# Optimization experiments

Hardware: AMD Instinct MI355X
Metric: run time of the kernel (lower is better)

## Reference

```python
import jax, jax.numpy as jnp
import numpy as np

Q, M, KLEN, B = 512, 512, 1024, 4
D, H, DH, G = 1024, 16, 64, 4
DG = D // G          # 256
EPS = 1e-6
SCALE = 1.0 / DH ** 0.5


def _group_ln(x, gamma, beta, n_group):
    # x: [L, B, D]; torch std is unbiased (ddof=1); note (x-mean)/(std+eps)
    L, b, d = x.shape
    xg = x.reshape(L, b, n_group, d // n_group)
    mean = xg.mean(-1, keepdims=True)
    std = jnp.std(xg, axis=-1, ddof=1, keepdims=True)
    out = ((xg - mean) / (std + EPS)).reshape(L, b, d)
    return gamma * out + beta


def _rel_shift(x):
    # x: [q, r, b, n]
    q, r = x.shape[0], x.shape[1]
    zero_pad = jnp.zeros((q, 1) + x.shape[2:], x.dtype)
    x_padded = jnp.concatenate([zero_pad, x], axis=1).reshape((r + 1, q) + x.shape[2:])
    return x_padded[1:].reshape(x.shape)


def setup_inputs() -> dict:
    key = jax.random.key(0)
    ks = jax.random.split(key, 14)
    p = lambda k, s: jax.random.normal(k, s, jnp.float32) * 0.02
    w = jax.random.normal(ks[0], (Q, B, D), jnp.float32)
    r = jax.random.normal(ks[1], (KLEN, 1, D), jnp.float32)
    mems = jax.random.normal(ks[2], (M, B, D), jnp.float32)
    r_w_bias = p(ks[3], (H, DH))
    r_r_bias = p(ks[4], (H, DH))
    gamma_q = jnp.ones((D,), jnp.float32); beta_q = jnp.zeros((D,), jnp.float32)
    gamma_kv = jnp.ones((D,), jnp.float32); beta_kv = jnp.zeros((D,), jnp.float32)
    Wq = p(ks[5], (G, DG, DG))       # grouped conv1d k=1: per-group [out,in]
    Wiq = p(ks[6], (DG, D))          # inter_q_net: conv1d groups=1 [out,in]
    Wk = p(ks[7], (D, D))
    Wv = p(ks[8], (D, D))
    Wr = p(ks[9], (G, DG, DG))       # r_net grouped (n_head*d_head == d_model)
    Wintra = p(ks[10], (G, DG, DG))  # intra_linear grouped conv
    Winter = p(ks[11], (DG, D))      # inter_linear nn.Linear weight
    i = jnp.arange(Q)[:, None]
    j = jnp.arange(KLEN)[None, :]
    attn_mask = (j > i + M)[:, :, None]  # [Q, KLEN, 1] bool, True = masked
    return dict(w=w, r=r, r_w_bias=r_w_bias, r_r_bias=r_r_bias, mems=mems,
                gamma_q=gamma_q, beta_q=beta_q, gamma_kv=gamma_kv, beta_kv=beta_kv,
                Wq=Wq, Wiq=Wiq, Wk=Wk, Wv=Wv, Wr=Wr, Wintra=Wintra, Winter=Winter,
                attn_mask=attn_mask)


def reference(w, r, r_w_bias, r_r_bias, mems, gamma_q, beta_q, gamma_kv, beta_kv,
              Wq, Wiq, Wk, Wv, Wr, Wintra, Winter, attn_mask):
    qlen, bsz, _ = w.shape
    rlen = r.shape[0]
    w_norm = _group_ln(w, gamma_q, beta_q, G)                       # [Q,B,D]
    kv = jnp.concatenate([mems, w], axis=0)
    kv_norm = gamma_kv * (kv - kv.mean(-1, keepdims=True)) / (
        jnp.std(kv, axis=-1, ddof=1, keepdims=True) + EPS) + beta_kv  # [K,B,D]

    # grouped 1x1 conv projections == per-group matmuls
    q_intra = jnp.einsum('qbgd,god->qbgo', w_norm.reshape(qlen, bsz, G, DG), Wq)
    q_global = jnp.einsum('qbd,od->qbo', w_norm, Wiq)               # [Q,B,DG]
    head_q = (q_intra + q_global[:, :, None, :]).reshape(qlen, bsz, H, DH)
    klen = kv_norm.shape[0]
    head_k = jnp.einsum('kbd,od->kbo', kv_norm, Wk).reshape(klen, bsz, H, DH)
    head_v = jnp.einsum('kbd,od->kbo', kv_norm, Wv).reshape(klen, bsz, H, DH)
    r_head_k = jnp.einsum('rgd,god->rgo', r[:, 0].reshape(rlen, G, DG), Wr)
    r_head_k = r_head_k.reshape(rlen, H, DH)                        # [R,H,DH]

    AC = jnp.einsum('ibnd,jbnd->ijbn', head_q + r_w_bias, head_k)
    BD = _rel_shift(jnp.einsum('ibnd,jnd->ijbn', head_q + r_r_bias, r_head_k))
    attn_score = (AC + BD) * SCALE                                  # [Q,K,B,H]
    attn_score = jnp.where(attn_mask[:, :, :, None], -jnp.inf, attn_score)
    attn_prob = jax.nn.softmax(attn_score, axis=1)
    attn_vec = jnp.einsum('ijbn,jbnd->ibnd', attn_prob, head_v)
    attn_out = attn_vec.reshape(qlen, bsz, D)

    inter = jnp.einsum('qbd,od->qbo', attn_out, Winter)             # [Q,B,DG]
    intra = jnp.einsum('qbgd,god->qbgo', attn_out.reshape(qlen, bsz, G, DG), Wintra)
    out = (intra + inter[:, :, None, :]).reshape(qlen, bsz, D)
    return w + out
```

## Files before the change

kernel.cpp:

```cpp
#include <hip/hip_runtime.h>
#include <math.h>

#define Q_LEN 512
#define M_LEN 512
#define KL    1024
#define BSZ   4
#define DM    1024
#define NH    16
#define DHD   64
#define NG    4
#define DGRP  256
#define RL    1024
#define LN_EPS 1e-6f
#define ATT_SCALE 0.125f

typedef short s16x8 __attribute__((ext_vector_type(8)));
typedef float f32x4 __attribute__((ext_vector_type(4)));

__device__ __forceinline__ float wave_sum64(float v) {
#pragma unroll
    for (int off = 32; off > 0; off >>= 1) v += __shfl_xor(v, off);
    return v;
}

__device__ __forceinline__ ushort f2bf(float f) {
    unsigned u = __float_as_uint(f);
    unsigned r = (u + 0x7fffu + ((u >> 16) & 1u)) >> 16;
    return (ushort)r;
}
__device__ __forceinline__ float bf2f(ushort u) {
    return __uint_as_float(((unsigned)u) << 16);
}

__global__ __launch_bounds__(256) void cast4_kernel(
    const float* p0, const float* p1, const float* p2, const float* p3,
    ushort* d0, ushort* d1, ushort* d2, ushort* d3)
{
    int bid = blockIdx.x;
    const float* s; ushort* d; int off;
    if      (bid < 1024) { s = p0; d = d0; off = bid; }
    else if (bid < 2048) { s = p1; d = d1; off = bid - 1024; }
    else if (bid < 3072) { s = p2; d = d2; off = bid - 2048; }
    else                 { s = p3; d = d3; off = bid - 3072; }
    int i = off * 1024 + threadIdx.x * 4;
    float4 v = *(const float4*)(s + i);
    ushort4 o;
    o.x = f2bf(v.x); o.y = f2bf(v.y); o.z = f2bf(v.z); o.w = f2bf(v.w);
    *(ushort4*)(d + i) = o;
}

__global__ __launch_bounds__(256) void augment_kernel(
    const float* __restrict__ Wg0, const float* __restrict__ Wf0, ushort* __restrict__ Wo0,
    const float* __restrict__ Wg1, const float* __restrict__ Wf1, ushort* __restrict__ Wo1)
{
    int bid = blockIdx.x;
    const float* Wg; const float* Wf; ushort* Wo; int off;
    if (bid < 1024) { Wg = Wg0; Wf = Wf0; Wo = Wo0; off = bid; }
    else            { Wg = Wg1; Wf = Wf1; Wo = Wo1; off = bid - 1024; }
    int idx = off * 1024 + threadIdx.x * 4;
    int g = idx >> 18;
    int o = (idx >> 10) & 255;
    int k = idx & 1023;
    float4 v = *(const float4*)(Wf + o * 1024 + k);
    if ((k >> 8) == g) {
        float4 vg = *(const float4*)(Wg + ((g * 256 + o) << 8) + (k & 255));
        v.x += vg.x; v.y += vg.y; v.z += vg.z; v.w += vg.w;
    }
    ushort4 u;
    u.x = f2bf(v.x); u.y = f2bf(v.y); u.z = f2bf(v.z); u.w = f2bf(v.w);
    *(ushort4*)(Wo + idx) = u;
}

__global__ __launch_bounds__(64) void group_ln_kernel(
    const float* __restrict__ w, const float* __restrict__ gamma,
    const float* __restrict__ beta, ushort* __restrict__ out)
{
    int bid = blockIdx.x;
    int g = bid & (NG - 1);
    long long row = bid >> 2;
    int t = threadIdx.x;
    long long base = row * DM + g * DGRP + t * 4;
    float4 x = *(const float4*)(w + base);
    float mean = wave_sum64(x.x + x.y + x.z + x.w) * (1.0f / 256.0f);
    float dx = x.x - mean, dy = x.y - mean, dz = x.z - mean, dw = x.w - mean;
    float ss = wave_sum64(dx * dx + dy * dy + dz * dz + dw * dw);
    float inv = 1.0f / (sqrtf(ss * (1.0f / 255.0f)) + LN_EPS);
    int db = g * DGRP + t * 4;
    float4 ga = *(const float4*)(gamma + db);
    float4 be = *(const float4*)(beta + db);
    ushort4 o;
    o.x = f2bf(ga.x * (dx * inv) + be.x);
    o.y = f2bf(ga.y * (dy * inv) + be.y);
    o.z = f2bf(ga.z * (dz * inv) + be.z);
    o.w = f2bf(ga.w * (dw * inv) + be.w);
    *(ushort4*)(out + base) = o;
}

__global__ __launch_bounds__(256) void kv_ln_kernel(
    const float* __restrict__ mems, const float* __restrict__ w,
    const float* __restrict__ gamma, const float* __restrict__ beta,
    ushort* __restrict__ out)
{
    int row = blockIdx.x;
    int k = row >> 2, b = row & 3;
    const float* src = (k < M_LEN) ? (mems + ((long long)k * BSZ + b) * DM)
                                   : (w + ((long long)(k - M_LEN) * BSZ + b) * DM);
    int t = threadIdx.x;
    float4 x = *(const float4*)(src + t * 4);
    __shared__ float red[4];
    float s = wave_sum64(x.x + x.y + x.z + x.w);
    int wv = t >> 6, ln = t & 63;
    if (ln == 0) red[wv] = s;
    __syncthreads();
    float mean = (red[0] + red[1] + red[2] + red[3]) * (1.0f / 1024.0f);
    float dx = x.x - mean, dy = x.y - mean, dz = x.z - mean, dw = x.w - mean;
    float ss = wave_sum64(dx * dx + dy * dy + dz * dz + dw * dw);
    __syncthreads();
    if (ln == 0) red[wv] = ss;
    __syncthreads();
    float var = (red[0] + red[1] + red[2] + red[3]) * (1.0f / 1023.0f);
    float inv = 1.0f / (sqrtf(var) + LN_EPS);
    int db = t * 4;
    float4 ga = *(const float4*)(gamma + db);
    float4 be = *(const float4*)(beta + db);
    ushort4 o;
    o.x = f2bf(ga.x * (dx * inv) + be.x);
    o.y = f2bf(ga.y * (dy * inv) + be.y);
    o.z = f2bf(ga.z * (dz * inv) + be.z);
    o.w = f2bf(ga.w * (dw * inv) + be.w);
    *(ushort4*)(out + (long long)row * DM + db) = o;
}

__global__ __launch_bounds__(256) void gemm128_bf16_nt(
    const ushort* __restrict__ A, int lda,
    const ushort* __restrict__ W, long long wZ, int ldw,
    ushort* __restrict__ Cb, long long cZ, int ldc, int K)
{
    int z = blockIdx.z;
    W += (long long)z * wZ;
    Cb += (long long)z * cZ;
    int m0 = blockIdx.y * 128, n0 = blockIdx.x * 128;
    int t = threadIdx.x, lane = t & 63, w = t >> 6;
    int wr = w >> 1, wc = w & 1;
    int fr = lane & 15, kq = (lane >> 4) * 8;
    int srow = t >> 1, scol = (t & 1) * 16;

    __shared__ __align__(16) ushort As[128][40];
    __shared__ __align__(16) ushort Ws[128][40];

    const ushort* Ar = A + (long long)(m0 + srow) * lda + scol;
    const ushort* Wr = W + (long long)(n0 + srow) * ldw + scol;

    f32x4 acc[16] = {};

    s16x8 a0 = *(const s16x8*)Ar, a1 = *(const s16x8*)(Ar + 8);
    s16x8 b0 = *(const s16x8*)Wr, b1 = *(const s16x8*)(Wr + 8);
    *(s16x8*)&As[srow][scol] = a0; *(s16x8*)&As[srow][scol + 8] = a1;
    *(s16x8*)&Ws[srow][scol] = b0; *(s16x8*)&Ws[srow][scol + 8] = b1;
    __syncthreads();

    for (int k0 = 0; k0 < K; k0 += 32) {
        bool more = (k0 + 32) < K;
        if (more) {
            a0 = *(const s16x8*)(Ar + k0 + 32); a1 = *(const s16x8*)(Ar + k0 + 40);
            b0 = *(const s16x8*)(Wr + k0 + 32); b1 = *(const s16x8*)(Wr + k0 + 40);
        }
        s16x8 af[4], bf_[4];
#pragma unroll
        for (int rb = 0; rb < 4; ++rb)
            af[rb] = *(const s16x8*)&As[wr * 64 + rb * 16 + fr][kq];
#pragma unroll
        for (int cb = 0; cb < 4; ++cb)
            bf_[cb] = *(const s16x8*)&Ws[wc * 64 + cb * 16 + fr][kq];
#pragma unroll
        for (int rb = 0; rb < 4; ++rb)
#pragma unroll
            for (int cb = 0; cb < 4; ++cb)
                acc[rb * 4 + cb] = __builtin_amdgcn_mfma_f32_16x16x32_bf16(
                    af[rb], bf_[cb], acc[rb * 4 + cb], 0, 0, 0);
        __syncthreads();
        if (more) {
            *(s16x8*)&As[srow][scol] = a0; *(s16x8*)&As[srow][scol + 8] = a1;
            *(s16x8*)&Ws[srow][scol] = b0; *(s16x8*)&Ws[srow][scol + 8] = b1;
            __syncthreads();
        }
    }

    int rbase = (lane >> 4) * 4;
#pragma unroll
    for (int rb = 0; rb < 4; ++rb)
#pragma unroll
        for (int p = 0; p < 4; ++p) {
            long long row = m0 + wr * 64 + rb * 16 + rbase + p;
            ushort* crow = Cb + row * ldc + n0 + wc * 64 + fr;
#pragma unroll
            for (int cb = 0; cb < 4; ++cb)
                crow[cb * 16] = f2bf(acc[rb * 4 + cb][p]);
        }
}

__global__ __launch_bounds__(256) void gemm_bf16_nt(
    const ushort* __restrict__ A, long long aZ, int lda,
    const ushort* __restrict__ W, long long wZ, int ldw,
    float* __restrict__ C, ushort* __restrict__ Cb, long long cZ, int ldc,
    int M, int N, int K,
    const float* __restrict__ add1, long long a1Z, int lda1,
    const float* __restrict__ add2, long long a2Z, int lda2)
{
    int z = blockIdx.z;
    A += (long long)z * aZ;
    W += (long long)z * wZ;
    if (C)  C += (long long)z * cZ;
    if (Cb) Cb += (long long)z * cZ;
    if (add1) add1 += (long long)z * a1Z;
    if (add2) add2 += (long long)z * a2Z;
    int m0 = blockIdx.y * 64, n0 = blockIdx.x * 64;
    int t = threadIdx.x;
    int lane = t & 63, wid = t >> 6;
    int wr = wid >> 1, wc = wid & 1;
    int srow = t >> 2, scol = (t & 3) * 16;
    int fr = lane & 15, kq = (lane >> 4) * 8;

    __shared__ __align__(16) ushort As[64][72];
    __shared__ __align__(16) ushort Ws[64][72];

    f32x4 acc00 = {}, acc01 = {}, acc10 = {}, acc11 = {};

    const ushort* Arow = A + (long long)(m0 + srow) * lda + scol;
    const ushort* Wrow = W + (long long)(n0 + srow) * ldw + scol;

    s16x8 ra0 = *(const s16x8*)Arow;
    s16x8 ra1 = *(const s16x8*)(Arow + 8);
    s16x8 rw0 = *(const s16x8*)Wrow;
    s16x8 rw1 = *(const s16x8*)(Wrow + 8);
    *(s16x8*)&As[srow][scol] = ra0; *(s16x8*)&As[srow][scol + 8] = ra1;
    *(s16x8*)&Ws[srow][scol] = rw0; *(s16x8*)&Ws[srow][scol + 8] = rw1;
    __syncthreads();

    for (int k0 = 0; k0 < K; k0 += 64) {
        bool hasNext = (k0 + 64) < K;
        if (hasNext) {
            ra0 = *(const s16x8*)(Arow + k0 + 64);
            ra1 = *(const s16x8*)(Arow + k0 + 72);
            rw0 = *(const s16x8*)(Wrow + k0 + 64);
            rw1 = *(const s16x8*)(Wrow + k0 + 72);
        }
#pragma unroll
        for (int kk = 0; kk < 64; kk += 32) {
            s16x8 a0 = *(const s16x8*)&As[wr * 32 + fr][kk + kq];
            s16x8 a1 = *(const s16x8*)&As[wr * 32 + 16 + fr][kk + kq];
            s16x8 b0 = *(const s16x8*)&Ws[wc * 32 + fr][kk + kq];
            s16x8 b1 = *(const s16x8*)&Ws[wc * 32 + 16 + fr][kk + kq];
            acc00 = __builtin_amdgcn_mfma_f32_16x16x32_bf16(a0, b0, acc00, 0, 0, 0);
            acc01 = __builtin_amdgcn_mfma_f32_16x16x32_bf16(a0, b1, acc01, 0, 0, 0);
            acc10 = __builtin_amdgcn_mfma_f32_16x16x32_bf16(a1, b0, acc10, 0, 0, 0);
            acc11 = __builtin_amdgcn_mfma_f32_16x16x32_bf16(a1, b1, acc11, 0, 0, 0);
        }
        __syncthreads();
        if (hasNext) {
            *(s16x8*)&As[srow][scol] = ra0; *(s16x8*)&As[srow][scol + 8] = ra1;
            *(s16x8*)&Ws[srow][scol] = rw0; *(s16x8*)&Ws[srow][scol + 8] = rw1;
            __syncthreads();
        }
    }

    int rbase = (lane >> 4) * 4;
#pragma unroll
    for (int p = 0; p < 4; ++p) {
        int mrow0 = wr * 32 + rbase + p;
        int mrow1 = mrow0 + 16;
        int ncol0 = wc * 32 + fr;
        int ncol1 = ncol0 + 16;
        float v00 = acc00[p], v01 = acc01[p], v10 = acc10[p], v11 = acc11[p];
        long long r0 = m0 + mrow0, r1 = m0 + mrow1;
        int c0 = n0 + ncol0, c1 = n0 + ncol1;
        if (add1) {
            v00 += add1[r0 * lda1 + c0]; v01 += add1[r0 * lda1 + c1];
            v10 += add1[r1 * lda1 + c0]; v11 += add1[r1 * lda1 + c1];
        }
        if (add2) {
            v00 += add2[r0 * lda2 + c0]; v01 += add2[r0 * lda2 + c1];
            v10 += add2[r1 * lda2 + c0]; v11 += add2[r1 * lda2 + c1];
        }
        if (Cb) {
            Cb[r0 * ldc + c0] = f2bf(v00); Cb[r0 * ldc + c1] = f2bf(v01);
            Cb[r1 * ldc + c0] = f2bf(v10); Cb[r1 * ldc + c1] = f2bf(v11);
        } else {
            C[r0 * ldc + c0] = v00; C[r0 * ldc + c1] = v01;
            C[r1 * ldc + c0] = v10; C[r1 * ldc + c1] = v11;
        }
    }
}

__global__ __launch_bounds__(256) void transpose_v_kernel(
    const ushort* __restrict__ vin, ushort* __restrict__ vout)
{
    __shared__ __align__(16) ushort T[64][72];
    int bn = blockIdx.y;
    int b = bn >> 4, n = bn & 15;
    int k0 = blockIdx.x * 64;
    int t = threadIdx.x;
    {
        int kr = t >> 2, dp = (t & 3) * 16;
        const ushort* sp = vin + (((long long)(k0 + kr)) * 4 + b) * DM + n * DHD + dp;
        *(s16x8*)&T[kr][dp] = *(const s16x8*)sp;
        *(s16x8*)&T[kr][dp + 8] = *(const s16x8*)(sp + 8);
    }
    __syncthreads();
    {
        int d = t >> 2, kp = (t & 3) * 16;
        ushort vals[16];
#pragma unroll
        for (int q = 0; q < 16; ++q) vals[q] = T[kp + q][d];
        ushort* dp = vout + ((long long)bn * DHD + d) * KL + k0 + kp;
        *(s16x8*)dp = *(const s16x8*)&vals[0];
        *(s16x8*)(dp + 8) = *(const s16x8*)&vals[8];
    }
}

__global__ __launch_bounds__(256) void corr_kernel(
    const ushort* __restrict__ r_hk, const float* __restrict__ rwb,
    const float* __restrict__ rrb, float* __restrict__ corr)
{
    int n = blockIdx.y;
    int k = blockIdx.x * 4 + (threadIdx.x >> 6);
    int d = threadIdx.x & 63;
    float diff = rrb[n * DHD + d] - rwb[n * DHD + d];
    float v = diff * bf2f(r_hk[(long long)k * DM + n * DHD + d]);
    v = wave_sum64(v);
    if (d == 0) corr[n * RL + k] = v;
}

__global__ __launch_bounds__(256) void attn_mfma_kernel(
    const ushort* __restrict__ hq, const ushort* __restrict__ hk,
    const ushort* __restrict__ hvT, const ushort* __restrict__ rhk,
    const float* __restrict__ corr, ushort* __restrict__ attn_out)
{
    __shared__ __align__(16) ushort Ks[2][64][72];
    __shared__ __align__(16) ushort VsT[2][64][72];
    __shared__ __align__(16) ushort RKs[128][72];
    __shared__ __align__(16) ushort BDs[64][128];
    __shared__ __align__(16) ushort Ps[64][64];

    int bh = blockIdx.y;
    int b = bh >> 4, n = bh & 15;
    int i0 = blockIdx.x * 64;
    int t = threadIdx.x;
    int lane = t & 63, w = t >> 6;
    int lr16 = lane & 15;
    int lk8 = (lane >> 4) * 8;
    int orow = (lane >> 4) * 4;
    int swzBD = ((lane >> 4) & 3) << 4;

    s16x8 qf0, qf1;
    {
        const ushort* qp = hq + (((long long)(i0 + w * 16 + lr16)) * 4 + b) * DM
                              + n * DHD + lk8;
        qf0 = *(const s16x8*)qp;
        qf1 = *(const s16x8*)(qp + 32);
    }

    f32x4 O[4] = {};
    float m_[4], l_[4];
#pragma unroll
    for (int r = 0; r < 4; ++r) { m_[r] = -INFINITY; l_[r] = 0.0f; }

    int nJ = ((i0 + 575) >> 6) + 1;
    if (nJ > 16) nJ = 16;
    int ka0 = 448 - i0;

    int srow = t >> 2, sdp = (t & 3) * 16;

    {
        const ushort* kp = hk + (((long long)srow) * 4 + b) * DM + n * DHD + sdp;
        *(s16x8*)&Ks[0][srow][sdp] = *(const s16x8*)kp;
        *(s16x8*)&Ks[0][srow][sdp + 8] = *(const s16x8*)(kp + 8);
        const ushort* vp = hvT + ((long long)bh * DHD + srow) * KL + sdp;
        *(s16x8*)&VsT[0][srow][sdp] = *(const s16x8*)vp;
        *(s16x8*)&VsT[0][srow][sdp + 8] = *(const s16x8*)(vp + 8);
        int rr = t >> 1, dp2 = (t & 1) * 32;
        int rabs = ka0 + rr;
        const ushort* rp = rhk + (long long)rabs * DM + n * DHD + dp2;
        int phys = rabs & 127;
#pragma unroll
        for (int q = 0; q < 4; ++q)
            *(s16x8*)&RKs[phys][dp2 + q * 8] = *(const s16x8*)(rp + q * 8);
    }
    __syncthreads();

    int cur = 0;
    for (int jt = 0; jt < nJ; ++jt) {
        int j0 = jt * 64;
        int ka = ka0 + j0;
        bool hasNext = (jt + 1) < nJ;

        s16x8 pk0 = {}, pk1 = {}, pv0 = {}, pv1 = {}, pr0 = {}, pr1 = {};
        if (hasNext) {
            int j0n = j0 + 64;
            const ushort* kp = hk + (((long long)(j0n + srow)) * 4 + b) * DM + n * DHD + sdp;
            pk0 = *(const s16x8*)kp;
            pk1 = *(const s16x8*)(kp + 8);
            const ushort* vp = hvT + ((long long)bh * DHD + srow) * KL + j0n + sdp;
            pv0 = *(const s16x8*)vp;
            pv1 = *(const s16x8*)(vp + 8);
            int rnew = ka + 128 + srow;
            if (rnew < RL) {
                const ushort* rp = rhk + (long long)rnew * DM + n * DHD + sdp;
                pr0 = *(const s16x8*)rp;
                pr1 = *(const s16x8*)(rp + 8);
            }
        }

        f32x4 ac[4] = {};
#pragma unroll
        for (int nb = 0; nb < 4; ++nb) {
            s16x8 kb0 = *(const s16x8*)&Ks[cur][nb * 16 + lr16][lk8];
            s16x8 kb1 = *(const s16x8*)&Ks[cur][nb * 16 + lr16][32 + lk8];
            ac[nb] = __builtin_amdgcn_mfma_f32_16x16x32_bf16(qf0, kb0, ac[nb], 0, 0, 0);
            ac[nb] = __builtin_amdgcn_mfma_f32_16x16x32_bf16(qf1, kb1, ac[nb], 0, 0, 0);
        }
        int nb0 = (jt == 0) ? 0 : 4;
        for (int nb = nb0; nb < 8; ++nb) {
            int kk = nb * 16 + lr16;
            int rabs = ka + kk;
            int phys = rabs & 127;
            f32x4 bd = {};
            s16x8 rb0 = *(const s16x8*)&RKs[phys][lk8];
            s16x8 rb1 = *(const s16x8*)&RKs[phys][32 + lk8];
            bd = __builtin_amdgcn_mfma_f32_16x16x32_bf16(qf0, rb0, bd, 0, 0, 0);
            bd = __builtin_amdgcn_mfma_f32_16x16x32_bf16(qf1, rb1, bd, 0, 0, 0);
            float cadd = (rabs < RL) ? corr[n * RL + rabs] : 0.0f;
            int colw = phys ^ swzBD;
#pragma unroll
            for (int reg = 0; reg < 4; ++reg)
                BDs[w * 16 + orow + reg][colw] = f2bf(bd[reg] + cadd);
        }
        if (jt == 0) __syncthreads();

        float pvv[4][4], rowm[4];
#pragma unroll
        for (int reg = 0; reg < 4; ++reg) {
            int il = w * 16 + orow + reg;
            int i = i0 + il;
            rowm[reg] = -INFINITY;
#pragma unroll
            for (int nb = 0; nb < 4; ++nb) {
                int jc = nb * 16 + lr16;
                int j = j0 + jc;
                float s = -INFINITY;
                if (j <= i + M_LEN) {
                    int phys = (j + 511 - i) & 127;
                    s = (ac[nb][reg] + bf2f(BDs[il][phys ^ swzBD])) * ATT_SCALE;
                }
                pvv[reg][nb] = s;
                rowm[reg] = fmaxf(rowm[reg], s);
            }
        }
#pragma unroll
        for (int st = 1; st <= 8; st <<= 1)
#pragma unroll
            for (int reg = 0; reg < 4; ++reg)
                rowm[reg] = fmaxf(rowm[reg], __shfl_xor(rowm[reg], st));
        float rs[4], alpha[4];
#pragma unroll
        for (int reg = 0; reg < 4; ++reg) {
            int il = w * 16 + orow + reg;
            float newm = fmaxf(m_[reg], rowm[reg]);
            alpha[reg] = __expf(m_[reg] - newm);
            m_[reg] = newm;
            rs[reg] = 0.0f;
#pragma unroll
            for (int nb = 0; nb < 4; ++nb) {
                float p = __expf(pvv[reg][nb] - newm);
                rs[reg] += p;
                int jc = nb * 16 + lr16;
                int colp = (((jc >> 3) ^ (il & 7)) << 3) | (jc & 7);
                Ps[il][colp] = f2bf(p);
            }
        }
#pragma unroll
        for (int st = 1; st <= 8; st <<= 1)
#pragma unroll
            for (int reg = 0; reg < 4; ++reg)
                rs[reg] += __shfl_xor(rs[reg], st);
#pragma unroll
        for (int reg = 0; reg < 4; ++reg) {
            l_[reg] = l_[reg] * alpha[reg] + rs[reg];
#pragma unroll
            for (int nb = 0; nb < 4; ++nb) O[nb][reg] *= alpha[reg];
        }

        {
            int prow = w * 16 + lr16;
            int rh = prow & 7;
#pragma unroll
            for (int kc = 0; kc < 2; ++kc) {
                int blk = kc * 4 + (lane >> 4);
                s16x8 pa = *(const s16x8*)&Ps[prow][(blk ^ rh) << 3];
#pragma unroll
                for (int nb = 0; nb < 4; ++nb) {
                    s16x8 vb = *(const s16x8*)&VsT[cur][nb * 16 + lr16][kc * 32 + lk8];
                    O[nb] = __builtin_amdgcn_mfma_f32_16x16x32_bf16(pa, vb, O[nb], 0, 0, 0);
                }
            }
        }

        if (hasNext) {
            *(s16x8*)&Ks[cur ^ 1][srow][sdp] = pk0;
            *(s16x8*)&Ks[cur ^ 1][srow][sdp + 8] = pk1;
            *(s16x8*)&VsT[cur ^ 1][srow][sdp] = pv0;
            *(s16x8*)&VsT[cur ^ 1][srow][sdp + 8] = pv1;
            int phys = (ka + 128 + srow) & 127;
            *(s16x8*)&RKs[phys][sdp] = pr0;
            *(s16x8*)&RKs[phys][sdp + 8] = pr1;
        }
        __syncthreads();
        cur ^= 1;
    }

#pragma unroll
    for (int reg = 0; reg < 4; ++reg) {
        int il = w * 16 + orow + reg;
        long long i = i0 + il;
        float inv = 1.0f / l_[reg];
#pragma unroll
        for (int nb = 0; nb < 4; ++nb)
            attn_out[(i * 4 + b) * DM + n * DHD + nb * 16 + lr16] = f2bf(O[nb][reg] * inv);
    }
}

extern "C" void kernel_launch(void* const* d_in, const int* in_sizes, int n_in,
                              void* d_out, int out_size, void* d_ws, size_t ws_size,
                              hipStream_t stream) {
    const float* w       = (const float*)d_in[0];
    const float* r       = (const float*)d_in[1];
    const float* rwb     = (const float*)d_in[2];
    const float* rrb     = (const float*)d_in[3];
    const float* mems    = (const float*)d_in[4];
    const float* gamma_q = (const float*)d_in[5];
    const float* beta_q  = (const float*)d_in[6];
    const float* gamma_kv= (const float*)d_in[7];
    const float* beta_kv = (const float*)d_in[8];
    const float* Wq      = (const float*)d_in[9];
    const float* Wiq     = (const float*)d_in[10];
    const float* Wk      = (const float*)d_in[11];
    const float* Wv      = (const float*)d_in[12];
    const float* Wr      = (const float*)d_in[13];
    const float* Wintra  = (const float*)d_in[14];
    const float* Winter  = (const float*)d_in[15];
    float* out = (float*)d_out;
    float* ws = (float*)d_ws;

    float* corr = ws;

    ushort* w_norm_bf  = (ushort*)(corr + 16384);
    ushort* kv_norm_bf = w_norm_bf + 2097152;
    ushort* head_q_bf  = kv_norm_bf + 4194304;
    ushort* head_k_bf  = head_q_bf + 2097152;
    ushort* head_v_bf  = head_k_bf + 4194304;
    ushort* head_vT_bf = head_v_bf + 4194304;
    ushort* r_hk_bf    = head_vT_bf + 4194304;
    ushort* attn_o_bf  = r_hk_bf + 1048576;
    ushort* r_bf       = attn_o_bf + 2097152;
    ushort* Wk_bf      = r_bf + 1048576;
    ushort* Wv_bf      = Wk_bf + 1048576;
    ushort* Wr_bf      = Wv_bf + 1048576;
    ushort* Wq_aug     = Wr_bf + 262144;
    ushort* Wo_aug     = Wq_aug + 1048576;

    group_ln_kernel<<<dim3(Q_LEN * BSZ * NG), 64, 0, stream>>>(w, gamma_q, beta_q, w_norm_bf);
    kv_ln_kernel<<<dim3(KL * BSZ), 256, 0, stream>>>(mems, w, gamma_kv, beta_kv, kv_norm_bf);

    cast4_kernel<<<dim3(3328), 256, 0, stream>>>(
        r, Wk, Wv, Wr, r_bf, Wk_bf, Wv_bf, Wr_bf);
    augment_kernel<<<dim3(2048), 256, 0, stream>>>(
        Wq, Wiq, Wq_aug, Wintra, Winter, Wo_aug);

    gemm128_bf16_nt<<<dim3(8, 32, 2), 256, 0, stream>>>(
        kv_norm_bf, DM, Wk_bf, 1048576, DM, head_k_bf, 4194304, DM, DM);
    transpose_v_kernel<<<dim3(16, 64), 256, 0, stream>>>(head_v_bf, head_vT_bf);

    gemm_bf16_nt<<<dim3(4, 32, 4), 256, 0, stream>>>(
        w_norm_bf, 0, DM, Wq_aug, 262144, DM, nullptr, head_q_bf, DGRP, DM,
        Q_LEN * BSZ, DGRP, DM, nullptr, 0, 0, rwb, DGRP, 0);
    gemm_bf16_nt<<<dim3(4, 16, 4), 256, 0, stream>>>(
        r_bf, DGRP, DM, Wr_bf, DGRP * DGRP, DGRP, nullptr, r_hk_bf, DGRP, DM,
        RL, DGRP, DGRP, nullptr, 0, 0, nullptr, 0, 0);

    corr_kernel<<<dim3(RL / 4, NH), 256, 0, stream>>>(r_hk_bf, rwb, rrb, corr);

    attn_mfma_kernel<<<dim3(Q_LEN / 64, BSZ * NH), 256, 0, stream>>>(
        head_q_bf, head_k_bf, head_vT_bf, r_hk_bf, corr, attn_o_bf);

    gemm_bf16_nt<<<dim3(4, 32, 4), 256, 0, stream>>>(
        attn_o_bf, 0, DM, Wo_aug, 262144, DM, out, nullptr, DGRP, DM,
        Q_LEN * BSZ, DGRP, DM, w, DGRP, DM, nullptr, 0, 0);
}
```

Baseline: 163.6 us.

## Split attention over key range with one-wave blocks and a merge kernel

```diff
diff --git a/kernel.cpp b/kernel.cpp
--- a/kernel.cpp
+++ b/kernel.cpp
@@ -331,129 +331,96 @@
     if (d == 0) corr[n * RL + k] = v;
 }
 
-__global__ __launch_bounds__(256) void attn_mfma_kernel(
+__global__ __launch_bounds__(64, 4) void attn_split_kernel(
     const ushort* __restrict__ hq, const ushort* __restrict__ hk,
     const ushort* __restrict__ hvT, const ushort* __restrict__ rhk,
-    const float* __restrict__ corr, ushort* __restrict__ attn_out)
-{
-    __shared__ __align__(16) ushort Ks[2][64][72];
-    __shared__ __align__(16) ushort VsT[2][64][72];
-    __shared__ __align__(16) ushort RKs[128][72];
-    __shared__ __align__(16) ushort BDs[64][128];
-    __shared__ __align__(16) ushort Ps[64][64];
-
+    const float* __restrict__ corr,
+    float* __restrict__ Op0, float* __restrict__ Op1, float* __restrict__ Ml)
+{
+    __shared__ __align__(16) ushort BDs[16][128];
+    __shared__ __align__(16) ushort Ps[16][64];
+
+    int bx = blockIdx.x;
+    int iw = bx >> 1, s = bx & 1;
     int bh = blockIdx.y;
     int b = bh >> 4, n = bh & 15;
-    int i0 = blockIdx.x * 64;
-    int t = threadIdx.x;
-    int lane = t & 63, w = t >> 6;
+    int i0 = iw * 16;
+    int lane = threadIdx.x;
     int lr16 = lane & 15;
-    int lk8 = (lane >> 4) * 8;
-    int orow = (lane >> 4) * 4;
-    int swzBD = ((lane >> 4) & 3) << 4;
-
-    s16x8 qf0, qf1;
-    {
-        const ushort* qp = hq + (((long long)(i0 + w * 16 + lr16)) * 4 + b) * DM
-                              + n * DHD + lk8;
-        qf0 = *(const s16x8*)qp;
-        qf1 = *(const s16x8*)(qp + 32);
-    }
+    int hi = lane >> 4;
+    int lk8 = hi * 8;
+    int orow = hi * 4;
+    int swzBD = (hi & 3) << 4;
+
+    const ushort* qp = hq + (((long long)(i0 + lr16)) * 4 + b) * DM + n * DHD + lk8;
+    s16x8 qf0 = *(const s16x8*)qp;
+    s16x8 qf1 = *(const s16x8*)(qp + 32);
 
     f32x4 O[4] = {};
     float m_[4], l_[4];
 #pragma unroll
     for (int r = 0; r < 4; ++r) { m_[r] = -INFINITY; l_[r] = 0.0f; }
 
-    int nJ = ((i0 + 575) >> 6) + 1;
+    int nJ = ((i0 + 527) >> 6) + 1;
     if (nJ > 16) nJ = 16;
-    int ka0 = 448 - i0;
-
-    int srow = t >> 2, sdp = (t & 3) * 16;
-
-    {
-        const ushort* kp = hk + (((long long)srow) * 4 + b) * DM + n * DHD + sdp;
-        *(s16x8*)&Ks[0][srow][sdp] = *(const s16x8*)kp;
-        *(s16x8*)&Ks[0][srow][sdp + 8] = *(const s16x8*)(kp + 8);
-        const ushort* vp = hvT + ((long long)bh * DHD + srow) * KL + sdp;
-        *(s16x8*)&VsT[0][srow][sdp] = *(const s16x8*)vp;
-        *(s16x8*)&VsT[0][srow][sdp + 8] = *(const s16x8*)(vp + 8);
-        int rr = t >> 1, dp2 = (t & 1) * 32;
-        int rabs = ka0 + rr;
-        const ushort* rp = rhk + (long long)rabs * DM + n * DHD + dp2;
-        int phys = rabs & 127;
-#pragma unroll
-        for (int q = 0; q < 4; ++q)
-            *(s16x8*)&RKs[phys][dp2 + q * 8] = *(const s16x8*)(rp + q * 8);
-    }
-    __syncthreads();
-
-    int cur = 0;
-    for (int jt = 0; jt < nJ; ++jt) {
+    int h = (nJ + 1) >> 1;
+    int jts = s ? h : 0, jte = s ? nJ : h;
+    int ka0 = 496 - i0;
+
+    for (int jt = jts; jt < jte; ++jt) {
         int j0 = jt * 64;
         int ka = ka0 + j0;
-        bool hasNext = (jt + 1) < nJ;
-
-        s16x8 pk0 = {}, pk1 = {}, pv0 = {}, pv1 = {}, pr0 = {}, pr1 = {};
-        if (hasNext) {
-            int j0n = j0 + 64;
-            const ushort* kp = hk + (((long long)(j0n + srow)) * 4 + b) * DM + n * DHD + sdp;
-            pk0 = *(const s16x8*)kp;
-            pk1 = *(const s16x8*)(kp + 8);
-            const ushort* vp = hvT + ((long long)bh * DHD + srow) * KL + j0n + sdp;
-            pv0 = *(const s16x8*)vp;
-            pv1 = *(const s16x8*)(vp + 8);
-            int rnew = ka + 128 + srow;
-            if (rnew < RL) {
-                const ushort* rp = rhk + (long long)rnew * DM + n * DHD + sdp;
-                pr0 = *(const s16x8*)rp;
-                pr1 = *(const s16x8*)(rp + 8);
-            }
-        }
 
         f32x4 ac[4] = {};
 #pragma unroll
         for (int nb = 0; nb < 4; ++nb) {
-            s16x8 kb0 = *(const s16x8*)&Ks[cur][nb * 16 + lr16][lk8];
-            s16x8 kb1 = *(const s16x8*)&Ks[cur][nb * 16 + lr16][32 + lk8];
+            const ushort* kp = hk + (((long long)(j0 + nb * 16 + lr16)) * 4 + b) * DM
+                                  + n * DHD + lk8;
+            s16x8 kb0 = *(const s16x8*)kp;
+            s16x8 kb1 = *(const s16x8*)(kp + 32);
             ac[nb] = __builtin_amdgcn_mfma_f32_16x16x32_bf16(qf0, kb0, ac[nb], 0, 0, 0);
             ac[nb] = __builtin_amdgcn_mfma_f32_16x16x32_bf16(qf1, kb1, ac[nb], 0, 0, 0);
         }
-        int nb0 = (jt == 0) ? 0 : 4;
+
+        int nb0 = (jt == jts) ? 0 : 4;
         for (int nb = nb0; nb < 8; ++nb) {
             int kk = nb * 16 + lr16;
             int rabs = ka + kk;
             int phys = rabs & 127;
+            s16x8 rb0 = {}, rb1 = {};
+            float cadd = 0.0f;
+            if (rabs < RL) {
+                const ushort* rp = rhk + (long long)rabs * DM + n * DHD + lk8;
+                rb0 = *(const s16x8*)rp;
+                rb1 = *(const s16x8*)(rp + 32);
+                cadd = corr[n * RL + rabs];
+            }
             f32x4 bd = {};
-            s16x8 rb0 = *(const s16x8*)&RKs[phys][lk8];
-            s16x8 rb1 = *(const s16x8*)&RKs[phys][32 + lk8];
             bd = __builtin_amdgcn_mfma_f32_16x16x32_bf16(qf0, rb0, bd, 0, 0, 0);
             bd = __builtin_amdgcn_mfma_f32_16x16x32_bf16(qf1, rb1, bd, 0, 0, 0);
-            float cadd = (rabs < RL) ? corr[n * RL + rabs] : 0.0f;
             int colw = phys ^ swzBD;
 #pragma unroll
             for (int reg = 0; reg < 4; ++reg)
-                BDs[w * 16 + orow + reg][colw] = f2bf(bd[reg] + cadd);
-        }
-        if (jt == 0) __syncthreads();
+                BDs[orow + reg][colw] = f2bf(bd[reg] + cadd);
+        }
 
         float pvv[4][4], rowm[4];
 #pragma unroll
         for (int reg = 0; reg < 4; ++reg) {
-            int il = w * 16 + orow + reg;
+            int il = orow + reg;
             int i = i0 + il;
             rowm[reg] = -INFINITY;
 #pragma unroll
             for (int nb = 0; nb < 4; ++nb) {
                 int jc = nb * 16 + lr16;
                 int j = j0 + jc;
-                float s = -INFINITY;
+                float sv = -INFINITY;
                 if (j <= i + M_LEN) {
                     int phys = (j + 511 - i) & 127;
-                    s = (ac[nb][reg] + bf2f(BDs[il][phys ^ swzBD])) * ATT_SCALE;
+                    sv = (ac[nb][reg] + bf2f(BDs[il][phys ^ swzBD])) * ATT_SCALE;
                 }
-                pvv[reg][nb] = s;
-                rowm[reg] = fmaxf(rowm[reg], s);
+                pvv[reg][nb] = sv;
+                rowm[reg] = fmaxf(rowm[reg], sv);
             }
         }
 #pragma unroll
@@ -464,7 +431,7 @@
         float rs[4], alpha[4];
 #pragma unroll
         for (int reg = 0; reg < 4; ++reg) {
-            int il = w * 16 + orow + reg;
+            int il = orow + reg;
             float newm = fmaxf(m_[reg], rowm[reg]);
             alpha[reg] = __expf(m_[reg] - newm);
             m_[reg] = newm;
@@ -491,42 +458,64 @@
         }
 
         {
-            int prow = w * 16 + lr16;
-            int rh = prow & 7;
+            int rh = lr16 & 7;
 #pragma unroll
             for (int kc = 0; kc < 2; ++kc) {
-                int blk = kc * 4 + (lane >> 4);
-                s16x8 pa = *(const s16x8*)&Ps[prow][(blk ^ rh) << 3];
+                int blk = kc * 4 + hi;
+                s16x8 pa = *(const s16x8*)&Ps[lr16][(blk ^ rh) << 3];
 #pragma unroll
                 for (int nb = 0; nb < 4; ++nb) {
-                    s16x8 vb = *(const s16x8*)&VsT[cur][nb * 16 + lr16][kc * 32 + lk8];
+                    const ushort* vp = hvT + ((long long)(bh * DHD + nb * 16 + lr16)) * KL
+                                           + j0 + kc * 32 + lk8;
+                    s16x8 vb = *(const s16x8*)vp;
                     O[nb] = __builtin_amdgcn_mfma_f32_16x16x32_bf16(pa, vb, O[nb], 0, 0, 0);
                 }
             }
         }
-
-        if (hasNext) {
-            *(s16x8*)&Ks[cur ^ 1][srow][sdp] = pk0;
-            *(s16x8*)&Ks[cur ^ 1][srow][sdp + 8] = pk1;
-            *(s16x8*)&VsT[cur ^ 1][srow][sdp] = pv0;
-            *(s16x8*)&VsT[cur ^ 1][srow][sdp + 8] = pv1;
-            int phys = (ka + 128 + srow) & 127;
-            *(s16x8*)&RKs[phys][sdp] = pr0;
-            *(s16x8*)&RKs[phys][sdp + 8] = pr1;
-        }
-        __syncthreads();
-        cur ^= 1;
-    }
-
+    }
+
+    float* Ob = s ? Op1 : Op0;
 #pragma unroll
     for (int reg = 0; reg < 4; ++reg) {
-        int il = w * 16 + orow + reg;
+        int il = orow + reg;
         long long i = i0 + il;
-        float inv = 1.0f / l_[reg];
 #pragma unroll
         for (int nb = 0; nb < 4; ++nb)
-            attn_out[(i * 4 + b) * DM + n * DHD + nb * 16 + lr16] = f2bf(O[nb][reg] * inv);
-    }
+            Ob[(i * 4 + b) * DM + n * DHD + nb * 16 + lr16] = O[nb][reg];
+    }
+    if (lr16 == 0) {
+#pragma unroll
+        for (int reg = 0; reg < 4; ++reg) {
+            int i = i0 + orow + reg;
+            long long ridx = ((long long)s * 32768 + ((i * 4 + b) * 16 + n)) * 2;
+            Ml[ridx] = m_[reg];
+            Ml[ridx + 1] = l_[reg];
+        }
+    }
+}
+
+__global__ __launch_bounds__(256) void merge_kernel(
+    const float* __restrict__ Op0, const float* __restrict__ Op1,
+    const float* __restrict__ Ml, ushort* __restrict__ outb)
+{
+    int gid = blockIdx.x * 256 + threadIdx.x;
+    int row = gid >> 4;
+    int d4 = (gid & 15) * 4;
+    float m0 = Ml[row * 2], l0 = Ml[row * 2 + 1];
+    float m1 = Ml[65536 + row * 2], l1 = Ml[65536 + row * 2 + 1];
+    float M = fmaxf(m0, m1);
+    float w0 = __expf(m0 - M), w1 = __expf(m1 - M);
+    float den = l0 * w0 + l1 * w1;
+    float s0 = w0 / den, s1 = w1 / den;
+    long long off = (long long)row * 64 + d4;
+    float4 o0 = *(const float4*)(Op0 + off);
+    float4 o1 = *(const float4*)(Op1 + off);
+    ushort4 o;
+    o.x = f2bf(o0.x * s0 + o1.x * s1);
+    o.y = f2bf(o0.y * s0 + o1.y * s1);
+    o.z = f2bf(o0.z * s0 + o1.z * s1);
+    o.w = f2bf(o0.w * s0 + o1.w * s1);
+    *(ushort4*)(outb + off) = o;
 }
 
 extern "C" void kernel_launch(void* const* d_in, const int* in_sizes, int n_in,
@@ -568,6 +557,10 @@
     ushort* Wq_aug     = Wr_bf + 262144;
     ushort* Wo_aug     = Wq_aug + 1048576;
 
+    float* Op0 = (float*)kv_norm_bf;
+    float* Op1 = (float*)head_v_bf;
+    float* Ml  = (float*)w_norm_bf;
+
     group_ln_kernel<<<dim3(Q_LEN * BSZ * NG), 64, 0, stream>>>(w, gamma_q, beta_q, w_norm_bf);
     kv_ln_kernel<<<dim3(KL * BSZ), 256, 0, stream>>>(mems, w, gamma_kv, beta_kv, kv_norm_bf);
 
@@ -589,8 +582,9 @@
 
     corr_kernel<<<dim3(RL / 4, NH), 256, 0, stream>>>(r_hk_bf, rwb, rrb, corr);
 
-    attn_mfma_kernel<<<dim3(Q_LEN / 64, BSZ * NH), 256, 0, stream>>>(
-        head_q_bf, head_k_bf, head_vT_bf, r_hk_bf, corr, attn_o_bf);
+    attn_split_kernel<<<dim3(64, 64), 64, 0, stream>>>(
+        head_q_bf, head_k_bf, head_vT_bf, r_hk_bf, corr, Op0, Op1, Ml);
+    merge_kernel<<<dim3(2048), 256, 0, stream>>>(Op0, Op1, Ml, attn_o_bf);
 
     gemm_bf16_nt<<<dim3(4, 32, 4), 256, 0, stream>>>(
         attn_o_bf, 0, DM, Wo_aug, 262144, DM, out, nullptr, DGRP, DM,
```

New measurement: 195.1 us. 1.19x slower.
